# Kernel optimization log

Hardware: AMD Instinct MI355X
Metric: run time of the kernel (lower is better)

The kernel has to match this reference:

```python
import jax, jax.numpy as jnp
import numpy as np

B, L, F, H, ZD, FX, FZ = 512, 1024, 38, 256, 4, 64, 32
HZ = FZ // 2  # hidden layer of feature_extra_z MLP


def setup_inputs() -> dict:
    key = jax.random.key(0)
    ks = jax.random.split(key, 22)
    g = lambda k, shape, s=0.05: jax.random.normal(k, shape, dtype=jnp.float32) * s
    return {
        'x': jax.random.normal(ks[0], (B, L, F), dtype=jnp.float32),
        'eps': jax.random.normal(ks[1], (L, B, ZD), dtype=jnp.float32),
        # feature_extra_x: MLPEmbedding(F -> FX), single linear + ReLU (dropout off in eval)
        'Wx': g(ks[2], (FX, F)), 'bx': jnp.zeros((FX,), jnp.float32),
        # feature_extra_z: MLPEmbedding(ZD -> FZ) with hidden [FZ//2]
        'Wz1': g(ks[3], (HZ, ZD)), 'bz1': jnp.zeros((HZ,), jnp.float32),
        'Wz2': g(ks[4], (FZ, HZ)), 'bz2': jnp.zeros((FZ,), jnp.float32),
        # phi_norm: NormalParam(H+FX -> ZD): loc linear + softplus(scale linear)
        'Wp_loc': g(ks[5], (ZD, H + FX)), 'bp_loc': jnp.zeros((ZD,), jnp.float32),
        'Wp_scale': g(ks[6], (ZD, H + FX)), 'bp_scale': jnp.zeros((ZD,), jnp.float32),
        # theta_norm_2: NormalParam(FZ+H -> F)
        'Wt_loc': g(ks[7], (F, FZ + H)), 'bt_loc': jnp.zeros((F,), jnp.float32),
        'Wt_scale': g(ks[8], (F, FZ + H)), 'bt_scale': jnp.zeros((F,), jnp.float32),
        # GRUCell(input=FX+FZ, hidden=H), torch layout: W_ih [3H, in], W_hh [3H, H]
        'W_ih': g(ks[9], (3 * H, FX + FZ)), 'W_hh': g(ks[10], (3 * H, H)),
        'b_ih': jnp.zeros((3 * H,), jnp.float32), 'b_hh': jnp.zeros((3 * H,), jnp.float32),
    }


def _gru_cell(xin, h, W_ih, W_hh, b_ih, b_hh):
    gi = xin @ W_ih.T + b_ih          # [B, 3H]
    gh = h @ W_hh.T + b_hh            # [B, 3H]
    i_r, i_z, i_n = jnp.split(gi, 3, axis=1)
    h_r, h_z, h_n = jnp.split(gh, 3, axis=1)
    r = jax.nn.sigmoid(i_r + h_r)
    zg = jax.nn.sigmoid(i_z + h_z)
    n = jnp.tanh(i_n + r * h_n)
    return (1.0 - zg) * n + zg * h


def reference(x, eps, Wx, bx, Wz1, bz1, Wz2, bz2,
              Wp_loc, bp_loc, Wp_scale, bp_scale,
              Wt_loc, bt_loc, Wt_scale, bt_scale,
              W_ih, W_hh, b_ih, b_hh):
    # precompute x features for all timesteps (eval mode: dropout is identity)
    fx = jax.nn.relu(jnp.einsum('blf,ef->ble', x, Wx) + bx)  # [B,L,FX]
    fx_t = jnp.transpose(fx, (1, 0, 2))                       # [L,B,FX]

    h0 = jnp.zeros((x.shape[0], H), x.dtype)

    def step(h, inp):
        fxt, epst = inp                                       # [B,FX], [B,ZD]
        # encode: phi_norm(cat(h, fx_t)) + reparameterized sample
        hx = jnp.concatenate([h, fxt], axis=1)                # [B,H+FX]
        z_loc = hx @ Wp_loc.T + bp_loc
        z_scale = jax.nn.softplus(hx @ Wp_scale.T + bp_scale)
        z = z_loc + z_scale * epst                            # [B,ZD]
        # feature_extra_z MLP
        fz = jax.nn.relu(z @ Wz1.T + bz1)
        fz = jax.nn.relu(fz @ Wz2.T + bz2)                    # [B,FZ]
        # decode: theta_norm_2(cat(fz, h)) -> x_loc
        zh = jnp.concatenate([fz, h], axis=1)                 # [B,FZ+H]
        x_loc = zh @ Wt_loc.T + bt_loc                        # [B,F]
        # recurrence
        h_new = _gru_cell(jnp.concatenate([fxt, fz], axis=1), h, W_ih, W_hh, b_ih, b_hh)
        return h_new, x_loc

    _, res = jax.lax.scan(step, h0, (fx_t, eps))              # res: [L,B,F]
    return jnp.transpose(res, (1, 0, 2))                      # [B,L,F]
```

## Files before the change

### kernel.cpp

```cpp
#include <hip/hip_runtime.h>
#include <hip/hip_fp16.h>

typedef unsigned short ushort_t;
typedef unsigned int uint_t;

#define BN 512
#define LN 1024
#define FN 38
#define HN 256
#define ZDN 4
#define FXN 64
#define FZN 32

#define NT 512
#define NWG 32
#define BT 16

#define RB 0
#define ZB 176
#define HB 352
#define IB 480
#define TB 528
#define PB 555
#define NENT 565

__device__ __forceinline__ ushort_t f2h(float f) { return __half_as_ushort(__float2half(f)); }
__device__ __forceinline__ float h2f(ushort_t u) { return __half2float(__ushort_as_half(u)); }
__device__ __forceinline__ uint_t pk2(float a, float b) {
    return (uint_t)f2h(a) | ((uint_t)f2h(b) << 16);
}
__device__ __forceinline__ float fsig(float v) { return 1.0f / (1.0f + __expf(-v)); }
__device__ __forceinline__ float ftanh(float v) { return 1.0f - 2.0f / (__expf(2.0f * v) + 1.0f); }
__device__ __forceinline__ float fsoftplus(float v) {
    return fmaxf(v, 0.0f) + __logf(1.0f + __expf(-fabsf(v)));
}

typedef _Float16 h8 __attribute__((ext_vector_type(8)));
typedef float f4 __attribute__((ext_vector_type(4)));
#define MFMA(A, B, C) __builtin_amdgcn_mfma_f32_16x16x32_f16((A), (B), (C), 0, 0, 0)
__device__ __forceinline__ h8 bch8(uint4 v) { return __builtin_bit_cast(h8, v); }

__global__ __launch_bounds__(256) void repack_frags(
    const float* __restrict__ W_ih, const float* __restrict__ W_hh,
    const float* __restrict__ Wt_loc,
    const float* __restrict__ Wp_loc, const float* __restrict__ Wp_scale,
    ushort_t* __restrict__ wfrag) {
    int idx = blockIdx.x * 256 + threadIdx.x;
    if (idx >= NENT * 512) return;
    int e = idx >> 9, r512 = idx & 511, ln = r512 >> 3, i = r512 & 7;
    int row = ln & 15, kl = ((ln >> 4) << 3) + i;
    float v = 0.0f;
    if (e < ZB) {
        int mt = e / 11, ks = e % 11, j = mt * 16 + row, ak = ks * 32 + kl;
        v = (ak < 256) ? W_hh[j * 256 + ak] : W_ih[j * 96 + ak - 256];
    } else if (e < HB) {
        int e2 = e - ZB, mt = e2 / 11, ks = e2 % 11, j = mt * 16 + row, ak = ks * 32 + kl;
        v = (ak < 256) ? W_hh[(256 + j) * 256 + ak] : W_ih[(256 + j) * 96 + ak - 256];
    } else if (e < IB) {
        int e2 = e - HB, mt = e2 / 8, ks = e2 % 8, j = mt * 16 + row;
        v = W_hh[(512 + j) * 256 + ks * 32 + kl];
    } else if (e < TB) {
        int e2 = e - IB, mt = e2 / 3, ksx = e2 % 3, j = mt * 16 + row;
        v = W_ih[(512 + j) * 96 + ksx * 32 + kl];
    } else if (e < PB) {
        int e2 = e - TB, mtt = e2 / 9, tks = e2 % 9, f = mtt * 16 + row;
        int col = (tks == 0) ? kl : 32 + (tks - 1) * 32 + kl;
        v = (f < FN) ? Wt_loc[f * 288 + col] : 0.0f;
    } else {
        int ks = e - PB, col = ks * 32 + kl;
        if (row < 4) v = Wp_loc[row * 320 + col];
        else if (row < 8) v = Wp_scale[(row - 4) * 320 + col];
    }
    wfrag[idx] = f2h(v);
}

__global__ __launch_bounds__(256) void fx_pre(const float* __restrict__ x,
                                              const float* __restrict__ Wx,
                                              const float* __restrict__ bx,
                                              ushort_t* __restrict__ fxbuf) {
    __shared__ float w[FXN][FN + 1];
    __shared__ float bxs[FXN];
    int t = threadIdx.x;
    for (int i = t; i < FXN * FN; i += 256) w[i / FN][i % FN] = Wx[i];
    if (t < FXN) bxs[t] = bx[t];
    __syncthreads();
    size_t id = (size_t)blockIdx.x * 256 + t;
    const float* xr = x + id * FN;
    float xv[FN];
#pragma unroll
    for (int f = 0; f < FN; ++f) xv[f] = xr[f];
    uint4* dst = (uint4*)(fxbuf + id * FXN);
#pragma unroll
    for (int e8 = 0; e8 < 8; ++e8) {
        float a[8];
#pragma unroll
        for (int u = 0; u < 8; ++u) {
            int e = e8 * 8 + u;
            float acc = bxs[e];
#pragma unroll
            for (int f = 0; f < FN; ++f) acc += xv[f] * w[e][f];
            a[u] = fmaxf(acc, 0.0f);
        }
        uint4 o;
        o.x = pk2(a[0], a[1]); o.y = pk2(a[2], a[3]);
        o.z = pk2(a[4], a[5]); o.w = pk2(a[6], a[7]);
        dst[e8] = o;
    }
}

#define AIDX(buf, ks) (((buf) * 11 + (ks)) * 512)

template <bool FXPRE>
__global__ __launch_bounds__(NT) void vrnn_mfma(
    const float* __restrict__ x, const float* __restrict__ eps,
    const float* __restrict__ Wx, const float* __restrict__ bx,
    const float* __restrict__ Wz1, const float* __restrict__ bz1,
    const float* __restrict__ Wz2, const float* __restrict__ bz2,
    const float* __restrict__ bp_loc, const float* __restrict__ bp_scale,
    const float* __restrict__ bt_loc,
    const float* __restrict__ b_ih, const float* __restrict__ b_hh,
    const ushort_t* __restrict__ wfrag, const ushort_t* __restrict__ fxbuf,
    float* __restrict__ out)
{
    __shared__ __attribute__((aligned(16))) ushort_t actf[2 * 11 * 512];
    __shared__ __attribute__((aligned(16))) uint_t phif[10 * 64 * 4];
    __shared__ __attribute__((aligned(16))) ushort_t wext[75 * 512];
    __shared__ float pp[8][16];
    __shared__ float bsr[HN], bsz[HN], bin_[HN], bhn_[HN];
    __shared__ float wz1s[16][ZDN], wz2s[FZN][16];
    __shared__ float bz1s[16], bz2s[FZN], btls[FN], bpls[ZDN], bpss[ZDN];
    __shared__ float wxs[FXN][FN + 2], bxs[FXN];

    const int t = threadIdx.x;
    const int w = t >> 6, ln = t & 63;
    const int b0 = blockIdx.x * BT;
    const uint4* WL = ((const uint4*)wfrag) + ln;

    {
        const uint_t* wfu = (const uint_t*)wfrag;
        for (int i = t; i < 10 * 256; i += NT) phif[i] = wfu[PB * 256 + i];
        uint2* we2 = (uint2*)wext;
        const uint2* ws2 = ((const uint2*)wfrag) + IB * 128;
        for (int i = t; i < 75 * 128; i += NT) we2[i] = ws2[i];
    }
    if (t < HN) {
        bsr[t] = b_ih[t] + b_hh[t];
        bsz[t] = b_ih[HN + t] + b_hh[HN + t];
        bin_[t] = b_ih[2 * HN + t];
        bhn_[t] = b_hh[2 * HN + t];
    }
    if (t >= 256 && t < 320) ((float*)wz1s)[t - 256] = Wz1[t - 256];
    for (int i = t; i < FZN * 16; i += NT) ((float*)wz2s)[i] = Wz2[i];
    if (t < 16) bz1s[t] = bz1[t];
    if (t >= 32 && t < 64) bz2s[t - 32] = bz2[t - 32];
    if (t >= 64 && t < 64 + FN) btls[t - 64] = bt_loc[t - 64];
    if (t >= 128 && t < 132) bpls[t - 128] = bp_loc[t - 128];
    if (t >= 160 && t < 164) bpss[t - 160] = bp_scale[t - 160];
    if (!FXPRE) {
        for (int i = t; i < FXN * FN; i += NT) wxs[i / FN][i % FN] = Wx[i];
        if (t >= 320 && t < 384) bxs[t - 320] = bx[t - 320];
    }
    for (int i = t; i < 8 * 512; i += NT) actf[AIDX(0, i >> 9) + (i & 511)] = 0;
    __syncthreads();
    if (t < 128) {
        int b = t >> 3, ch = t & 7;
        int dst = AIDX(0, 8 + (ch >> 2)) + ((ch & 3) * 16 + b) * 8;
        if (FXPRE) {
            uint4 v = ((const uint4*)fxbuf)[((size_t)(b0 + b) * LN) * 8 + ch];
            *(uint4*)&actf[dst] = v;
        } else {
            const float* xr = x + ((size_t)(b0 + b) * LN) * FN;
            uint_t o[4];
#pragma unroll
            for (int p = 0; p < 4; ++p) {
                float a0 = bxs[ch * 8 + 2 * p], a1 = bxs[ch * 8 + 2 * p + 1];
#pragma unroll
                for (int f = 0; f < FN; ++f) {
                    float xv = xr[f];
                    a0 += xv * wxs[ch * 8 + 2 * p][f];
                    a1 += xv * wxs[ch * 8 + 2 * p + 1][f];
                }
                o[p] = pk2(fmaxf(a0, 0.0f), fmaxf(a1, 0.0f));
            }
            *(uint4*)&actf[dst] = make_uint4(o[0], o[1], o[2], o[3]);
        }
    }
    __syncthreads();

    const int mtA = 2 * w, mtB = 2 * w + 1;

#pragma unroll 1
    for (int l = 0; l < LN; ++l) {
        const int cur = l & 1, nxt = cur ^ 1;

        float4 pfe = {0, 0, 0, 0};
        if (t >= 256 && t < 384)
            pfe = *(const float4*)&eps[((size_t)l * BN + b0 + ((t - 256) >> 3)) * ZDN];

        f4 ra0 = {0,0,0,0}, rb0 = {0,0,0,0}, za0 = {0,0,0,0}, zb0 = {0,0,0,0};
        f4 na0 = {0,0,0,0}, nb0 = {0,0,0,0}, ia0 = {0,0,0,0}, ib0 = {0,0,0,0};
        f4 tp = {0,0,0,0};

        uint4 rac = WL[(RB + mtA * 11 + 0) * 64], rbc = WL[(RB + mtB * 11 + 0) * 64];
        uint4 zac = WL[(ZB + mtA * 11 + 0) * 64], zbc = WL[(ZB + mtB * 11 + 0) * 64];
        uint4 ran = WL[(RB + mtA * 11 + 1) * 64], rbn = WL[(RB + mtB * 11 + 1) * 64];
        uint4 zan = WL[(ZB + mtA * 11 + 1) * 64], zbn = WL[(ZB + mtB * 11 + 1) * 64];
        uint4 hac = WL[(HB + mtA * 8 + 0) * 64],  hbc = WL[(HB + mtB * 8 + 0) * 64];
        uint4 han = WL[(HB + mtA * 8 + 1) * 64],  hbn = WL[(HB + mtB * 8 + 1) * 64];

#pragma unroll
        for (int ks = 0; ks < 10; ++ks) {
            h8 B = *(const h8*)&actf[AIDX(cur, ks) + ln * 8];
            ra0 = MFMA(bch8(rac), B, ra0);
            rac = ran; if (ks < 9) ran = WL[(RB + mtA * 11 + ks + 2) * 64];
            rb0 = MFMA(bch8(rbc), B, rb0);
            rbc = rbn; if (ks < 9) rbn = WL[(RB + mtB * 11 + ks + 2) * 64];
            za0 = MFMA(bch8(zac), B, za0);
            zac = zan; if (ks < 9) zan = WL[(ZB + mtA * 11 + ks + 2) * 64];
            zb0 = MFMA(bch8(zbc), B, zb0);
            zbc = zbn; if (ks < 9) zbn = WL[(ZB + mtB * 11 + ks + 2) * 64];
            if (ks < 8) {
                na0 = MFMA(bch8(hac), B, na0);
                hac = han; if (ks < 6) han = WL[(HB + mtA * 8 + ks + 2) * 64];
                nb0 = MFMA(bch8(hbc), B, nb0);
                hbc = hbn; if (ks < 6) hbn = WL[(HB + mtB * 8 + ks + 2) * 64];
            } else {
                h8 wA = *(const h8*)&wext[(mtA * 3 + (ks - 8)) * 512 + ln * 8];
                h8 wB = *(const h8*)&wext[(mtB * 3 + (ks - 8)) * 512 + ln * 8];
                ia0 = MFMA(wA, B, ia0);
                ib0 = MFMA(wB, B, ib0);
            }
            if (w < 3) {
                if (ks < 8) {
                    h8 wt = *(const h8*)&wext[(48 + w * 9 + ks + 1) * 512 + ln * 8];
                    tp = MFMA(wt, B, tp);
                }
            } else if (w == 3) {
                uint4 pa = *(const uint4*)&phif[(ks * 64 + ln) * 4];
                tp = MFMA(bch8(pa), B, tp);
            }
        }
        if (w == 3 && (ln >> 4) < 2) {
#pragma unroll
            for (int q = 0; q < 4; ++q) pp[(ln >> 4) * 4 + q][ln & 15] = tp[q];
        }
        __syncthreads();

        if (t >= 256 && t < 384) {
            int tid = t - 256, b = tid >> 3, part = tid & 7;
            float ez[4] = {pfe.x, pfe.y, pfe.z, pfe.w};
            float zz[4];
#pragma unroll
            for (int c = 0; c < 4; ++c)
                zz[c] = pp[c][b] + bpls[c] + fsoftplus(pp[4 + c][b] + bpss[c]) * ez[c];
            float f1v[16];
#pragma unroll
            for (int k = 0; k < 16; ++k) {
                float a = bz1s[k];
#pragma unroll
                for (int c = 0; c < 4; ++c) a += zz[c] * wz1s[k][c];
                f1v[k] = fmaxf(a, 0.0f);
            }
            float v4[4];
#pragma unroll
            for (int oq = 0; oq < 4; ++oq) {
                int o = part * 4 + oq;
                float acc = bz2s[o];
#pragma unroll
                for (int k = 0; k < 16; ++k) acc += f1v[k] * wz2s[o][k];
                v4[oq] = fmaxf(acc, 0.0f);
            }
            uint2 pk; pk.x = pk2(v4[0], v4[1]); pk.y = pk2(v4[2], v4[3]);
            int dst = AIDX(cur, 10) + ((part >> 1) * 16 + b) * 8 + (part & 1) * 4;
            *(uint2*)&actf[dst] = pk;
        } else if (t >= 384) {
            int tid = t - 384, b = tid >> 3, ch = tid & 7;
            int lp = (l + 1 < LN) ? l + 1 : LN - 1;
            int dst = AIDX(nxt, 8 + (ch >> 2)) + ((ch & 3) * 16 + b) * 8;
            if (FXPRE) {
                uint4 v = ((const uint4*)fxbuf)[((size_t)(b0 + b) * LN + lp) * 8 + ch];
                *(uint4*)&actf[dst] = v;
            } else {
                const float* xr = x + ((size_t)(b0 + b) * LN + lp) * FN;
                uint_t o[4];
#pragma unroll
                for (int p = 0; p < 4; ++p) {
                    float a0 = bxs[ch * 8 + 2 * p], a1 = bxs[ch * 8 + 2 * p + 1];
#pragma unroll
                    for (int f = 0; f < FN; ++f) {
                        float xv = xr[f];
                        a0 += xv * wxs[ch * 8 + 2 * p][f];
                        a1 += xv * wxs[ch * 8 + 2 * p + 1][f];
                    }
                    o[p] = pk2(fmaxf(a0, 0.0f), fmaxf(a1, 0.0f));
                }
                *(uint4*)&actf[dst] = make_uint4(o[0], o[1], o[2], o[3]);
            }
        }
        __syncthreads();

        {
            h8 B = *(const h8*)&actf[AIDX(cur, 10) + ln * 8];
            ra0 = MFMA(bch8(rac), B, ra0);
            rb0 = MFMA(bch8(rbc), B, rb0);
            za0 = MFMA(bch8(zac), B, za0);
            zb0 = MFMA(bch8(zbc), B, zb0);
            h8 wA = *(const h8*)&wext[(mtA * 3 + 2) * 512 + ln * 8];
            h8 wB = *(const h8*)&wext[(mtB * 3 + 2) * 512 + ln * 8];
            ia0 = MFMA(wA, B, ia0);
            ib0 = MFMA(wB, B, ib0);
            if (w < 3) {
                h8 wt = *(const h8*)&wext[(48 + w * 9 + 0) * 512 + ln * 8];
                tp = MFMA(wt, B, tp);
            }
        }

#define PW(RACC, ZACC, NACC, IACC, MTL) do {                                        \
        int jb = (2 * w + (MTL)) * 16 + ((ln >> 4) << 2);                           \
        int abase = (((jb >> 3) & 3) * 16 + (ln & 15)) * 8 + (jb & 7);              \
        uint2 ho2 = *(const uint2*)&actf[AIDX(cur, jb >> 5) + abase];               \
        float ho[4] = { h2f((ushort_t)ho2.x), h2f((ushort_t)(ho2.x >> 16)),         \
                        h2f((ushort_t)ho2.y), h2f((ushort_t)(ho2.y >> 16)) };       \
        float hn4[4];                                                               \
        _Pragma("unroll")                                                           \
        for (int q = 0; q < 4; ++q) {                                               \
            float r_ = fsig((RACC)[q] + bsr[jb + q]);                               \
            float z_ = fsig((ZACC)[q] + bsz[jb + q]);                               \
            float n_ = ftanh((IACC)[q] + bin_[jb + q] + r_ * ((NACC)[q] + bhn_[jb + q])); \
            hn4[q] = (1.0f - z_) * n_ + z_ * ho[q];                                 \
        }                                                                           \
        uint2 hw2; hw2.x = pk2(hn4[0], hn4[1]); hw2.y = pk2(hn4[2], hn4[3]);        \
        *(uint2*)&actf[AIDX(nxt, jb >> 5) + abase] = hw2;                           \
    } while (0)

        PW(ra0, za0, na0, ia0, 0);
        PW(rb0, zb0, nb0, ib0, 1);
#undef PW

        if (w < 3) {
            int bb = b0 + (ln & 15);
            float* op = out + ((size_t)bb * LN + l) * FN;
#pragma unroll
            for (int q = 0; q < 4; ++q) {
                int f = w * 16 + ((ln >> 4) << 2) + q;
                if (f < FN) op[f] = tp[q] + btls[f];
            }
        }
        __syncthreads();
    }
}

extern "C" void kernel_launch(void* const* d_in, const int* in_sizes, int n_in,
                              void* d_out, int out_size, void* d_ws, size_t ws_size,
                              hipStream_t stream) {
    const float* x        = (const float*)d_in[0];
    const float* eps      = (const float*)d_in[1];
    const float* Wx       = (const float*)d_in[2];
    const float* bx       = (const float*)d_in[3];
    const float* Wz1      = (const float*)d_in[4];
    const float* bz1      = (const float*)d_in[5];
    const float* Wz2      = (const float*)d_in[6];
    const float* bz2      = (const float*)d_in[7];
    const float* Wp_loc   = (const float*)d_in[8];
    const float* bp_loc   = (const float*)d_in[9];
    const float* Wp_scale = (const float*)d_in[10];
    const float* bp_scale = (const float*)d_in[11];
    const float* Wt_loc   = (const float*)d_in[12];
    const float* bt_loc   = (const float*)d_in[13];
    const float* W_ih     = (const float*)d_in[16];
    const float* W_hh     = (const float*)d_in[17];
    const float* b_ih     = (const float*)d_in[18];
    const float* b_hh     = (const float*)d_in[19];
    float* out = (float*)d_out;

    const size_t wfS = (size_t)NENT * 512;
    const size_t fxS = (size_t)BN * LN * FXN;

    ushort_t* wfrag = (ushort_t*)d_ws;
    ushort_t* fxbuf = wfrag + wfS;

    repack_frags<<<(int)((wfS + 255) / 256), 256, 0, stream>>>(
        W_ih, W_hh, Wt_loc, Wp_loc, Wp_scale, wfrag);

    if (ws_size >= (wfS + fxS) * sizeof(ushort_t)) {
        fx_pre<<<BN * LN / 256, 256, 0, stream>>>(x, Wx, bx, fxbuf);
        vrnn_mfma<true><<<NWG, NT, 0, stream>>>(
            x, eps, Wx, bx, Wz1, bz1, Wz2, bz2, bp_loc, bp_scale, bt_loc,
            b_ih, b_hh, wfrag, fxbuf, out);
    } else {
        vrnn_mfma<false><<<NWG, NT, 0, stream>>>(
            x, eps, Wx, bx, Wz1, bz1, Wz2, bz2, bp_loc, bp_scale, bt_loc,
            b_ih, b_hh, wfrag, (const ushort_t*)nullptr, out);
    }
}
```

Measured before the change: 9.684 ms.

## Move fx-chunk MFMAs after the z stage and keep hidden state in registers

```diff
diff --git a/kernel.cpp b/kernel.cpp
--- a/kernel.cpp
+++ b/kernel.cpp
@@ -189,6 +189,15 @@
 
     const int mtA = 2 * w, mtB = 2 * w + 1;
 
+    float hA[4] = {0, 0, 0, 0}, hB[4] = {0, 0, 0, 0};
+
+    uint4 rac = WL[(RB + mtA * 11 + 0) * 64], rbc = WL[(RB + mtB * 11 + 0) * 64];
+    uint4 zac = WL[(ZB + mtA * 11 + 0) * 64], zbc = WL[(ZB + mtB * 11 + 0) * 64];
+    uint4 ran = WL[(RB + mtA * 11 + 1) * 64], rbn = WL[(RB + mtB * 11 + 1) * 64];
+    uint4 zan = WL[(ZB + mtA * 11 + 1) * 64], zbn = WL[(ZB + mtB * 11 + 1) * 64];
+    uint4 hac = WL[(HB + mtA * 8 + 0) * 64],  hbc = WL[(HB + mtB * 8 + 0) * 64];
+    uint4 han = WL[(HB + mtA * 8 + 1) * 64],  hbn = WL[(HB + mtB * 8 + 1) * 64];
+
 #pragma unroll 1
     for (int l = 0; l < LN; ++l) {
         const int cur = l & 1, nxt = cur ^ 1;
@@ -201,48 +210,40 @@
         f4 na0 = {0,0,0,0}, nb0 = {0,0,0,0}, ia0 = {0,0,0,0}, ib0 = {0,0,0,0};
         f4 tp = {0,0,0,0};
 
-        uint4 rac = WL[(RB + mtA * 11 + 0) * 64], rbc = WL[(RB + mtB * 11 + 0) * 64];
-        uint4 zac = WL[(ZB + mtA * 11 + 0) * 64], zbc = WL[(ZB + mtB * 11 + 0) * 64];
-        uint4 ran = WL[(RB + mtA * 11 + 1) * 64], rbn = WL[(RB + mtB * 11 + 1) * 64];
-        uint4 zan = WL[(ZB + mtA * 11 + 1) * 64], zbn = WL[(ZB + mtB * 11 + 1) * 64];
-        uint4 hac = WL[(HB + mtA * 8 + 0) * 64],  hbc = WL[(HB + mtB * 8 + 0) * 64];
-        uint4 han = WL[(HB + mtA * 8 + 1) * 64],  hbn = WL[(HB + mtB * 8 + 1) * 64];
-
-#pragma unroll
-        for (int ks = 0; ks < 10; ++ks) {
+#pragma unroll
+        for (int ks = 0; ks < 8; ++ks) {
             h8 B = *(const h8*)&actf[AIDX(cur, ks) + ln * 8];
             ra0 = MFMA(bch8(rac), B, ra0);
-            rac = ran; if (ks < 9) ran = WL[(RB + mtA * 11 + ks + 2) * 64];
+            rac = ran; ran = WL[(RB + mtA * 11 + ks + 2) * 64];
             rb0 = MFMA(bch8(rbc), B, rb0);
-            rbc = rbn; if (ks < 9) rbn = WL[(RB + mtB * 11 + ks + 2) * 64];
+            rbc = rbn; rbn = WL[(RB + mtB * 11 + ks + 2) * 64];
             za0 = MFMA(bch8(zac), B, za0);
-            zac = zan; if (ks < 9) zan = WL[(ZB + mtA * 11 + ks + 2) * 64];
+            zac = zan; zan = WL[(ZB + mtA * 11 + ks + 2) * 64];
             zb0 = MFMA(bch8(zbc), B, zb0);
-            zbc = zbn; if (ks < 9) zbn = WL[(ZB + mtB * 11 + ks + 2) * 64];
-            if (ks < 8) {
-                na0 = MFMA(bch8(hac), B, na0);
-                hac = han; if (ks < 6) han = WL[(HB + mtA * 8 + ks + 2) * 64];
-                nb0 = MFMA(bch8(hbc), B, nb0);
-                hbc = hbn; if (ks < 6) hbn = WL[(HB + mtB * 8 + ks + 2) * 64];
-            } else {
-                h8 wA = *(const h8*)&wext[(mtA * 3 + (ks - 8)) * 512 + ln * 8];
-                h8 wB = *(const h8*)&wext[(mtB * 3 + (ks - 8)) * 512 + ln * 8];
-                ia0 = MFMA(wA, B, ia0);
-                ib0 = MFMA(wB, B, ib0);
-            }
+            zbc = zbn; zbn = WL[(ZB + mtB * 11 + ks + 2) * 64];
+            na0 = MFMA(bch8(hac), B, na0);
+            hac = han; if (ks < 6) han = WL[(HB + mtA * 8 + ks + 2) * 64];
+            nb0 = MFMA(bch8(hbc), B, nb0);
+            hbc = hbn; if (ks < 6) hbn = WL[(HB + mtB * 8 + ks + 2) * 64];
             if (w < 3) {
-                if (ks < 8) {
-                    h8 wt = *(const h8*)&wext[(48 + w * 9 + ks + 1) * 512 + ln * 8];
-                    tp = MFMA(wt, B, tp);
-                }
+                h8 wt = *(const h8*)&wext[(48 + w * 9 + ks + 1) * 512 + ln * 8];
+                tp = MFMA(wt, B, tp);
             } else if (w == 3) {
                 uint4 pa = *(const uint4*)&phif[(ks * 64 + ln) * 4];
                 tp = MFMA(bch8(pa), B, tp);
             }
         }
-        if (w == 3 && (ln >> 4) < 2) {
-#pragma unroll
-            for (int q = 0; q < 4; ++q) pp[(ln >> 4) * 4 + q][ln & 15] = tp[q];
+        if (w == 3) {
+#pragma unroll
+            for (int ks = 8; ks < 10; ++ks) {
+                h8 B = *(const h8*)&actf[AIDX(cur, ks) + ln * 8];
+                uint4 pa = *(const uint4*)&phif[(ks * 64 + ln) * 4];
+                tp = MFMA(bch8(pa), B, tp);
+            }
+            if ((ln >> 4) < 2) {
+#pragma unroll
+                for (int q = 0; q < 4; ++q) pp[(ln >> 4) * 4 + q][ln & 15] = tp[q];
+            }
         }
         __syncthreads();
 
@@ -297,6 +298,23 @@
                 *(uint4*)&actf[dst] = make_uint4(o[0], o[1], o[2], o[3]);
             }
         }
+#pragma unroll
+        for (int kx = 0; kx < 2; ++kx) {
+            int ks = 8 + kx;
+            h8 B = *(const h8*)&actf[AIDX(cur, ks) + ln * 8];
+            ra0 = MFMA(bch8(rac), B, ra0);
+            rac = ran; if (kx == 0) ran = WL[(RB + mtA * 11 + 10) * 64];
+            rb0 = MFMA(bch8(rbc), B, rb0);
+            rbc = rbn; if (kx == 0) rbn = WL[(RB + mtB * 11 + 10) * 64];
+            za0 = MFMA(bch8(zac), B, za0);
+            zac = zan; if (kx == 0) zan = WL[(ZB + mtA * 11 + 10) * 64];
+            zb0 = MFMA(bch8(zbc), B, zb0);
+            zbc = zbn; if (kx == 0) zbn = WL[(ZB + mtB * 11 + 10) * 64];
+            h8 wA = *(const h8*)&wext[(mtA * 3 + kx) * 512 + ln * 8];
+            h8 wB = *(const h8*)&wext[(mtB * 3 + kx) * 512 + ln * 8];
+            ia0 = MFMA(wA, B, ia0);
+            ib0 = MFMA(wB, B, ib0);
+        }
         __syncthreads();
 
         {
@@ -315,26 +333,31 @@
             }
         }
 
-#define PW(RACC, ZACC, NACC, IACC, MTL) do {                                        \
+        rac = WL[(RB + mtA * 11 + 0) * 64]; rbc = WL[(RB + mtB * 11 + 0) * 64];
+        zac = WL[(ZB + mtA * 11 + 0) * 64]; zbc = WL[(ZB + mtB * 11 + 0) * 64];
+        ran = WL[(RB + mtA * 11 + 1) * 64]; rbn = WL[(RB + mtB * 11 + 1) * 64];
+        zan = WL[(ZB + mtA * 11 + 1) * 64]; zbn = WL[(ZB + mtB * 11 + 1) * 64];
+        hac = WL[(HB + mtA * 8 + 0) * 64];  hbc = WL[(HB + mtB * 8 + 0) * 64];
+        han = WL[(HB + mtA * 8 + 1) * 64];  hbn = WL[(HB + mtB * 8 + 1) * 64];
+
+#define PW(RACC, ZACC, NACC, IACC, MTL, HARR) do {                                  \
         int jb = (2 * w + (MTL)) * 16 + ((ln >> 4) << 2);                           \
         int abase = (((jb >> 3) & 3) * 16 + (ln & 15)) * 8 + (jb & 7);              \
-        uint2 ho2 = *(const uint2*)&actf[AIDX(cur, jb >> 5) + abase];               \
-        float ho[4] = { h2f((ushort_t)ho2.x), h2f((ushort_t)(ho2.x >> 16)),         \
-                        h2f((ushort_t)ho2.y), h2f((ushort_t)(ho2.y >> 16)) };       \
         float hn4[4];                                                               \
         _Pragma("unroll")                                                           \
         for (int q = 0; q < 4; ++q) {                                               \
             float r_ = fsig((RACC)[q] + bsr[jb + q]);                               \
             float z_ = fsig((ZACC)[q] + bsz[jb + q]);                               \
             float n_ = ftanh((IACC)[q] + bin_[jb + q] + r_ * ((NACC)[q] + bhn_[jb + q])); \
-            hn4[q] = (1.0f - z_) * n_ + z_ * ho[q];                                 \
+            hn4[q] = (1.0f - z_) * n_ + z_ * (HARR)[q];                             \
+            (HARR)[q] = hn4[q];                                                     \
         }                                                                           \
         uint2 hw2; hw2.x = pk2(hn4[0], hn4[1]); hw2.y = pk2(hn4[2], hn4[3]);        \
         *(uint2*)&actf[AIDX(nxt, jb >> 5) + abase] = hw2;                           \
     } while (0)
 
-        PW(ra0, za0, na0, ia0, 0);
-        PW(rb0, zb0, nb0, ib0, 1);
+        PW(ra0, za0, na0, ia0, 0, hA);
+        PW(rb0, zb0, nb0, ib0, 1, hB);
 #undef PW
 
         if (w < 3) {
```

Result: slower. 10.78 ms (+11.3%).

## Compute z-MLP in wave 3 via shuffles, drop a barrier, keep h in fp32 registers

Applied to the files above, without the earlier changes.

```diff
diff --git a/kernel.cpp b/kernel.cpp
--- a/kernel.cpp
+++ b/kernel.cpp
@@ -125,7 +125,6 @@
     __shared__ __attribute__((aligned(16))) ushort_t actf[2 * 11 * 512];
     __shared__ __attribute__((aligned(16))) uint_t phif[10 * 64 * 4];
     __shared__ __attribute__((aligned(16))) ushort_t wext[75 * 512];
-    __shared__ float pp[8][16];
     __shared__ float bsr[HN], bsz[HN], bin_[HN], bhn_[HN];
     __shared__ float wz1s[16][ZDN], wz2s[FZN][16];
     __shared__ float bz1s[16], bz2s[FZN], btls[FN], bpls[ZDN], bpss[ZDN];
@@ -189,13 +188,15 @@
 
     const int mtA = 2 * w, mtB = 2 * w + 1;
 
+    float hA[4] = {0, 0, 0, 0}, hB[4] = {0, 0, 0, 0};
+
 #pragma unroll 1
     for (int l = 0; l < LN; ++l) {
         const int cur = l & 1, nxt = cur ^ 1;
 
         float4 pfe = {0, 0, 0, 0};
-        if (t >= 256 && t < 384)
-            pfe = *(const float4*)&eps[((size_t)l * BN + b0 + ((t - 256) >> 3)) * ZDN];
+        if (w == 3)
+            pfe = *(const float4*)&eps[((size_t)l * BN + b0 + (ln & 15)) * ZDN];
 
         f4 ra0 = {0,0,0,0}, rb0 = {0,0,0,0}, za0 = {0,0,0,0}, zb0 = {0,0,0,0};
         f4 na0 = {0,0,0,0}, nb0 = {0,0,0,0}, ia0 = {0,0,0,0}, ib0 = {0,0,0,0};
@@ -240,19 +241,18 @@
                 tp = MFMA(bch8(pa), B, tp);
             }
         }
-        if (w == 3 && (ln >> 4) < 2) {
-#pragma unroll
-            for (int q = 0; q < 4; ++q) pp[(ln >> 4) * 4 + q][ln & 15] = tp[q];
-        }
-        __syncthreads();
-
-        if (t >= 256 && t < 384) {
-            int tid = t - 256, b = tid >> 3, part = tid & 7;
-            float ez[4] = {pfe.x, pfe.y, pfe.z, pfe.w};
+
+        if (w == 3) {
+            int b = ln & 15, s = ln >> 4;
+            float l0 = __shfl(tp[0], b), l1 = __shfl(tp[1], b);
+            float l2 = __shfl(tp[2], b), l3 = __shfl(tp[3], b);
+            float s0 = __shfl(tp[0], 16 + b), s1 = __shfl(tp[1], 16 + b);
+            float s2 = __shfl(tp[2], 16 + b), s3 = __shfl(tp[3], 16 + b);
             float zz[4];
-#pragma unroll
-            for (int c = 0; c < 4; ++c)
-                zz[c] = pp[c][b] + bpls[c] + fsoftplus(pp[4 + c][b] + bpss[c]) * ez[c];
+            zz[0] = l0 + bpls[0] + fsoftplus(s0 + bpss[0]) * pfe.x;
+            zz[1] = l1 + bpls[1] + fsoftplus(s1 + bpss[1]) * pfe.y;
+            zz[2] = l2 + bpls[2] + fsoftplus(s2 + bpss[2]) * pfe.z;
+            zz[3] = l3 + bpls[3] + fsoftplus(s3 + bpss[3]) * pfe.w;
             float f1v[16];
 #pragma unroll
             for (int k = 0; k < 16; ++k) {
@@ -261,18 +261,19 @@
                 for (int c = 0; c < 4; ++c) a += zz[c] * wz1s[k][c];
                 f1v[k] = fmaxf(a, 0.0f);
             }
-            float v4[4];
-#pragma unroll
-            for (int oq = 0; oq < 4; ++oq) {
-                int o = part * 4 + oq;
+            float v8[8];
+#pragma unroll
+            for (int u = 0; u < 8; ++u) {
+                int o = s * 8 + u;
                 float acc = bz2s[o];
 #pragma unroll
                 for (int k = 0; k < 16; ++k) acc += f1v[k] * wz2s[o][k];
-                v4[oq] = fmaxf(acc, 0.0f);
-            }
-            uint2 pk; pk.x = pk2(v4[0], v4[1]); pk.y = pk2(v4[2], v4[3]);
-            int dst = AIDX(cur, 10) + ((part >> 1) * 16 + b) * 8 + (part & 1) * 4;
-            *(uint2*)&actf[dst] = pk;
+                v8[u] = fmaxf(acc, 0.0f);
+            }
+            uint4 pk;
+            pk.x = pk2(v8[0], v8[1]); pk.y = pk2(v8[2], v8[3]);
+            pk.z = pk2(v8[4], v8[5]); pk.w = pk2(v8[6], v8[7]);
+            *(uint4*)&actf[AIDX(cur, 10) + ln * 8] = pk;
         } else if (t >= 384) {
             int tid = t - 384, b = tid >> 3, ch = tid & 7;
             int lp = (l + 1 < LN) ? l + 1 : LN - 1;
@@ -315,37 +316,36 @@
             }
         }
 
-#define PW(RACC, ZACC, NACC, IACC, MTL) do {                                        \
+        if (w < 3) {
+            int bb = b0 + (ln & 15);
+            float* op = out + ((size_t)bb * LN + l) * FN;
+#pragma unroll
+            for (int q = 0; q < 4; ++q) {
+                int f = w * 16 + ((ln >> 4) << 2) + q;
+                if (f < FN) op[f] = tp[q] + btls[f];
+            }
+        }
+
+#define PW(RACC, ZACC, NACC, IACC, MTL, HARR) do {                                  \
         int jb = (2 * w + (MTL)) * 16 + ((ln >> 4) << 2);                           \
         int abase = (((jb >> 3) & 3) * 16 + (ln & 15)) * 8 + (jb & 7);              \
-        uint2 ho2 = *(const uint2*)&actf[AIDX(cur, jb >> 5) + abase];               \
-        float ho[4] = { h2f((ushort_t)ho2.x), h2f((ushort_t)(ho2.x >> 16)),         \
-                        h2f((ushort_t)ho2.y), h2f((ushort_t)(ho2.y >> 16)) };       \
         float hn4[4];                                                               \
         _Pragma("unroll")                                                           \
         for (int q = 0; q < 4; ++q) {                                               \
             float r_ = fsig((RACC)[q] + bsr[jb + q]);                               \
             float z_ = fsig((ZACC)[q] + bsz[jb + q]);                               \
             float n_ = ftanh((IACC)[q] + bin_[jb + q] + r_ * ((NACC)[q] + bhn_[jb + q])); \
-            hn4[q] = (1.0f - z_) * n_ + z_ * ho[q];                                 \
+            hn4[q] = (1.0f - z_) * n_ + z_ * (HARR)[q];                             \
+            (HARR)[q] = hn4[q];                                                     \
         }                                                                           \
         uint2 hw2; hw2.x = pk2(hn4[0], hn4[1]); hw2.y = pk2(hn4[2], hn4[3]);        \
         *(uint2*)&actf[AIDX(nxt, jb >> 5) + abase] = hw2;                           \
     } while (0)
 
-        PW(ra0, za0, na0, ia0, 0);
-        PW(rb0, zb0, nb0, ib0, 1);
+        PW(ra0, za0, na0, ia0, 0, hA);
+        PW(rb0, zb0, nb0, ib0, 1, hB);
 #undef PW
 
-        if (w < 3) {
-            int bb = b0 + (ln & 15);
-            float* op = out + ((size_t)bb * LN + l) * FN;
-#pragma unroll
-            for (int q = 0; q < 4; ++q) {
-                int f = w * 16 + ((ln >> 4) << 2) + q;
-                if (f < FN) op[f] = tp[q] + btls[f];
-            }
-        }
         __syncthreads();
     }
 }
```

Result: slower. 10.17 ms (+5.0%).
